# Optimization experiments

Hardware: AMD Instinct MI355X
Metric: run time of the kernel (lower is better)

The kernel has to match this reference:

```python
import jax, jax.numpy as jnp
import numpy as np

T, B, D, H = 256, 64, 1024, 1024


def _linear_params(key, fan_in, shape_w, shape_b):
    kw, kb = jax.random.split(key)
    bound = 1.0 / np.sqrt(fan_in)
    W = jax.random.uniform(kw, shape_w, jnp.float32, -bound, bound)
    b = jax.random.uniform(kb, shape_b, jnp.float32, -bound, bound)
    return W, b


def setup_inputs() -> dict:
    key = jax.random.key(0)
    ks = jax.random.split(key, 6)
    x = jax.random.normal(ks[0], (T, B, D), jnp.float32)
    hidden = jnp.zeros((B, H), jnp.float32)
    cell = jnp.zeros((B, H), jnp.float32)
    W_in, b_in = _linear_params(ks[1], D, (H, D), (H,))
    W_hid, b_hid = _linear_params(ks[2], H, (H, H), (H,))
    # 4 gates (i, f, g, o), each with an x-path and h-path hidden->hidden Linear
    Wx_g, bx_g = _linear_params(ks[3], H, (4, H, H), (4, H))
    Wh_g, bh_g = _linear_params(ks[4], H, (4, H, H), (4, H))
    return {"x": x, "hidden": hidden, "cell": cell,
            "W_in": W_in, "b_in": b_in, "W_hid": W_hid, "b_hid": b_hid,
            "Wx_g": Wx_g, "bx_g": bx_g, "Wh_g": Wh_g, "bh_g": bh_g}


def reference(x, hidden, cell, W_in, b_in, W_hid, b_hid, Wx_g, bx_g, Wh_g, bh_g):
    # input_layer / hidden_layer projections, then 4 gate Linears per path,
    # mirroring the many-small-Linear LSTM cell of the torch module.
    def step(carry, x_t):
        h, c = carry
        x2h = x_t @ W_in.T + b_in          # [B, H]
        h2h = h @ W_hid.T + b_hid          # [B, H]
        g = (jnp.einsum('ghk,bk->gbh', Wx_g, x2h) + bx_g[:, None, :]
             + jnp.einsum('ghk,bk->gbh', Wh_g, h2h) + bh_g[:, None, :])  # [4, B, H]
        i = jax.nn.sigmoid(g[0])
        f = jax.nn.sigmoid(g[1])
        gg = jnp.tanh(g[2])
        o = jax.nn.sigmoid(g[3])
        c_new = f * c + i * gg
        h_new = o * jnp.tanh(c_new)
        return (h_new, c_new), None

    (h, c), _ = jax.lax.scan(step, (hidden, cell), x)
    return (h, c)
```

## Files before the change

### kernel.cpp

```cpp
#include <hip/hip_runtime.h>

typedef __attribute__((ext_vector_type(8))) short short8;
typedef __attribute__((ext_vector_type(4))) float f32x4;

#define SEQ_BLOCKS 64

__device__ __forceinline__ unsigned short f2bf(float f) {
  unsigned u = __float_as_uint(f);
  u = u + 0x7fffu + ((u >> 16) & 1u);
  return (unsigned short)(u >> 16);
}
__device__ __forceinline__ unsigned short f2h(float f) {
  _Float16 h = (_Float16)f;
  unsigned short r;
  __builtin_memcpy(&r, &h, 2);
  return r;
}
__device__ __forceinline__ float h2f(unsigned short u) {
  _Float16 h;
  __builtin_memcpy(&h, &u, 2);
  return (float)h;
}
__device__ __forceinline__ void gload16(const void* g, void* l) {
  __builtin_amdgcn_global_load_lds(
      (const __attribute__((address_space(1))) unsigned int*)g,
      (__attribute__((address_space(3))) unsigned int*)l, 16, 0, 0);
}
__device__ __forceinline__ float fast_sigmoid(float x) {
  return 1.0f / (1.0f + __expf(-x));
}
__device__ __forceinline__ float fast_tanh(float x) {
  return 2.0f / (1.0f + __expf(-2.0f * x)) - 1.0f;
}

__global__ void k_conv_bf16(const float* __restrict__ in, unsigned short* __restrict__ out) {
  size_t i = ((size_t)blockIdx.x * 256 + threadIdx.x) * 4;
  float4 v = *(const float4*)(in + i);
  unsigned short o[4] = {f2bf(v.x), f2bf(v.y), f2bf(v.z), f2bf(v.w)};
  *(uint2*)(out + i) = *(const uint2*)o;
}

__global__ void k_h0t(const float* __restrict__ hidden, unsigned short* __restrict__ hT) {
  int sb = blockIdx.x;
  int row = threadIdx.x >> 2, c4 = (threadIdx.x & 3) * 4;
  float4 v = *(const float4*)(hidden + (size_t)row * 1024 + sb * 16 + c4);
  unsigned short o[4] = {f2bf(v.x), f2bf(v.y), f2bf(v.z), f2bf(v.w)};
  unsigned long long u;
  __builtin_memcpy(&u, o, 8);
  *(unsigned long long*)(hT + (size_t)sb * 1024 + row * 16 + c4) = u;
}

__global__ void k_transpose(const float* __restrict__ in, unsigned short* __restrict__ out,
                            int R, int C) {
  __shared__ float tile[32][33];
  int bx = blockIdx.x * 32, by = blockIdx.y * 32;
  int tx = threadIdx.x & 31, ty = threadIdx.x >> 5;
  for (int i = 0; i < 32; i += 8)
    tile[ty + i][tx] = in[(size_t)(by + ty + i) * C + bx + tx];
  __syncthreads();
  for (int i = 0; i < 32; i += 8)
    out[(size_t)(bx + ty + i) * R + by + tx] = f2bf(tile[tx][ty + i]);
}

template<int OUTMODE>
__global__ __launch_bounds__(256) void k_gemm_bt(
    const unsigned short* __restrict__ A, const unsigned short* __restrict__ B,
    unsigned short* __restrict__ C, const float* __restrict__ bias,
    int M, int N, int K) {
  __shared__ unsigned short As[128 * 32];
  __shared__ unsigned short Bs[128 * 32];
  const int tid = threadIdx.x;
  const int wv = tid >> 6, l = tid & 63;
  const int m0 = blockIdx.y * 128, n0 = blockIdx.x * 128;
  const int wr = (wv >> 1) * 64, wc = (wv & 1) * 64;
  f32x4 acc[4][4] = {};
  for (int k0 = 0; k0 < K; k0 += 32) {
#pragma unroll
    for (int j = 0; j < 2; ++j) {
      int c = wv * 128 + j * 64 + l;
      int row = c >> 2, kc = (c & 3) * 8;
      gload16(A + (size_t)(m0 + row) * K + k0 + kc, (char*)As + c * 16);
      gload16(B + (size_t)(n0 + row) * K + k0 + kc, (char*)Bs + c * 16);
    }
    __syncthreads();
    short8 af[4], bfr[4];
#pragma unroll
    for (int rf = 0; rf < 4; ++rf)
      af[rf] = *(const short8*)(As + (wr + rf * 16 + (l & 15)) * 32 + (l >> 4) * 8);
#pragma unroll
    for (int cf = 0; cf < 4; ++cf)
      bfr[cf] = *(const short8*)(Bs + (wc + cf * 16 + (l & 15)) * 32 + (l >> 4) * 8);
#pragma unroll
    for (int rf = 0; rf < 4; ++rf)
#pragma unroll
      for (int cf = 0; cf < 4; ++cf)
        acc[rf][cf] = __builtin_amdgcn_mfma_f32_16x16x32_bf16(af[rf], bfr[cf], acc[rf][cf], 0, 0, 0);
    __syncthreads();
  }
#pragma unroll
  for (int cf = 0; cf < 4; ++cf) {
    int col = n0 + wc + cf * 16 + (l & 15);
    float bv = bias ? bias[col] : 0.0f;
#pragma unroll
    for (int rf = 0; rf < 4; ++rf) {
#pragma unroll
      for (int i = 0; i < 4; ++i) {
        int row = m0 + wr + rf * 16 + (l >> 4) * 4 + i;
        float v = acc[rf][cf][i] + bv;
        if (OUTMODE == 0) {
          C[(size_t)row * N + col] = f2bf(v);
        } else {
          int t = row >> 6, b = row & 63;
          int g = col >> 10, c = col & 1023;
          size_t idx = (size_t)(t * 64 + (c >> 4)) * 4096 + (g * 64 + b) * 16 + (c & 15);
          C[idx] = f2h(v);
        }
      }
    }
  }
}

__global__ void k_bias(const float* __restrict__ Wxg, const float* __restrict__ bxg,
                       const float* __restrict__ b_in, const float* __restrict__ Whg,
                       const float* __restrict__ bhg, const float* __restrict__ b_hid,
                       float* __restrict__ gbias) {
  int col = blockIdx.x * 64 + (threadIdx.x >> 2);
  int p = threadIdx.x & 3;
  const float* wx = Wxg + (size_t)col * 1024;
  const float* wh = Whg + (size_t)col * 1024;
  float s = 0.f;
  for (int k = p * 256; k < p * 256 + 256; ++k)
    s += wx[k] * b_in[k] + wh[k] * b_hid[k];
  s += __shfl_down(s, 2, 4);
  s += __shfl_down(s, 1, 4);
  if (p == 0) gbias[col] = s + bxg[col] + bhg[col];
}

__global__ __launch_bounds__(256, 1) void k_lstm_seq(
    const unsigned short* __restrict__ GX2,
    const unsigned short* __restrict__ Whc,
    const float* __restrict__ cell,
    unsigned short* __restrict__ hstep,
    float* __restrict__ out,
    unsigned* __restrict__ flags) {
  __shared__ float pbuf[34816];
  const int tid = threadIdx.x;
  const int wv = tid >> 6, l = tid & 63;
  const int bid = blockIdx.x;
  const int a = l & 15, q = l >> 4;

  short8 w[4][8];
#pragma unroll
  for (int ct = 0; ct < 4; ++ct)
#pragma unroll
    for (int u = 0; u < 8; ++u)
      w[ct][u] = *(const short8*)(
          Whc + (size_t)(ct * 1024 + bid * 16 + a) * 1024 + wv * 256 + u * 32 + q * 8);

  const int eb = tid >> 2;
  const int ej = (tid & 3) * 4;
  float c_reg[4];
  {
    float4 c4 = *(const float4*)(cell + (size_t)eb * 1024 + bid * 16 + ej);
    c_reg[0] = c4.x; c_reg[1] = c4.y; c_reg[2] = c4.z; c_reg[3] = c4.w;
  }

  const size_t abase = (size_t)(wv * 16 + (q >> 1)) * 1024 + a * 16 + (q & 1) * 8;
  const unsigned* pollp = flags + wv * 32 + a;

  for (int t = 0; t < 256; ++t) {
    const unsigned short* chunk = GX2 + ((size_t)t * 64 + bid) * 4096;
    unsigned long long gxu[4];
#pragma unroll
    for (int g = 0; g < 4; ++g)
      gxu[g] = *(const unsigned long long*)(chunk + (g * 64 + eb) * 16 + ej);

    if (t > 0) {
      const unsigned tgt = (unsigned)t;
      for (;;) {
        unsigned v = __hip_atomic_load(pollp, __ATOMIC_RELAXED, __HIP_MEMORY_SCOPE_AGENT);
        if (__all((int)(v >= tgt))) break;
        __builtin_amdgcn_s_sleep(1);
      }
      __builtin_amdgcn_fence(__ATOMIC_ACQUIRE, "workgroup");
      __builtin_amdgcn_sched_barrier(0);
    }

    const unsigned short* hb = hstep + ((size_t)t << 16) + abase;
    short8 afr[4][8];
#pragma unroll
    for (int u = 0; u < 8; ++u)
#pragma unroll
      for (int rt = 0; rt < 4; ++rt)
        afr[rt][u] = *(const short8*)(hb + u * 2048 + rt * 256);

    f32x4 acc[4][4] = {};
#pragma unroll
    for (int u = 0; u < 8; ++u)
#pragma unroll
      for (int rt = 0; rt < 4; ++rt)
#pragma unroll
        for (int ct = 0; ct < 4; ++ct)
          acc[rt][ct] = __builtin_amdgcn_mfma_f32_16x16x32_bf16(afr[rt][u], w[ct][u],
                                                                acc[rt][ct], 0, 0, 0);

    const int pb = (t & 1) * 17408 + wv * 4352;
#pragma unroll
    for (int rt = 0; rt < 4; ++rt)
#pragma unroll
      for (int ct = 0; ct < 4; ++ct) {
        int gc = a * 4 + ct;
        int b0 = (rt * 16 + q * 4) ^ ((((gc) >> 3) & 3) << 2);
        *(f32x4*)&pbuf[pb + gc * 68 + b0] = acc[rt][ct];
      }
    __syncthreads();

    const int pr = (t & 1) * 17408;
    float sg[4][4];
#pragma unroll
    for (int g = 0; g < 4; ++g) {
      unsigned short gx4[4];
      __builtin_memcpy(gx4, &gxu[g], 8);
#pragma unroll
      for (int i = 0; i < 4; ++i) {
        int gc = (ej + i) * 4 + g;
        int bx = eb ^ ((((gc) >> 3) & 3) << 2);
        float s = pbuf[pr + 0 * 4352 + gc * 68 + bx] + pbuf[pr + 1 * 4352 + gc * 68 + bx] +
                  pbuf[pr + 2 * 4352 + gc * 68 + bx] + pbuf[pr + 3 * 4352 + gc * 68 + bx];
        sg[g][i] = s + h2f(gx4[i]);
      }
    }
    float hnew[4];
#pragma unroll
    for (int i = 0; i < 4; ++i) {
      float ig = fast_sigmoid(sg[0][i]);
      float fg = fast_sigmoid(sg[1][i]);
      float gg = fast_tanh(sg[2][i]);
      float og = fast_sigmoid(sg[3][i]);
      c_reg[i] = fg * c_reg[i] + ig * gg;
      hnew[i] = og * fast_tanh(c_reg[i]);
    }

    if (t == 255) {
      float4 h4 = {hnew[0], hnew[1], hnew[2], hnew[3]};
      float4 c4 = {c_reg[0], c_reg[1], c_reg[2], c_reg[3]};
      *(float4*)(out + (size_t)eb * 1024 + bid * 16 + ej) = h4;
      *(float4*)(out + 65536 + (size_t)eb * 1024 + bid * 16 + ej) = c4;
    } else {
      unsigned short hs[4] = {f2bf(hnew[0]), f2bf(hnew[1]), f2bf(hnew[2]), f2bf(hnew[3])};
      unsigned long long hv;
      __builtin_memcpy(&hv, hs, 8);
      __hip_atomic_store(
          (unsigned long long*)(hstep + ((size_t)(t + 1) << 16) + (size_t)bid * 1024 +
                                eb * 16 + ej),
          hv, __ATOMIC_RELAXED, __HIP_MEMORY_SCOPE_AGENT);
      asm volatile("s_waitcnt vmcnt(0)" ::: "memory");
      __syncthreads();
      if (tid == 0)
        __hip_atomic_store(&flags[(bid >> 4) * 32 + (bid & 15)], (unsigned)(t + 1),
                           __ATOMIC_RELAXED, __HIP_MEMORY_SCOPE_AGENT);
    }
  }
}

extern "C" void kernel_launch(void* const* d_in, const int* in_sizes, int n_in,
                              void* d_out, int out_size, void* d_ws, size_t ws_size,
                              hipStream_t stream) {
  const float* x      = (const float*)d_in[0];
  const float* hidden = (const float*)d_in[1];
  const float* cell   = (const float*)d_in[2];
  const float* W_in   = (const float*)d_in[3];
  const float* b_in   = (const float*)d_in[4];
  const float* W_hid  = (const float*)d_in[5];
  const float* b_hid  = (const float*)d_in[6];
  const float* Wx_g   = (const float*)d_in[7];
  const float* bx_g   = (const float*)d_in[8];
  const float* Wh_g   = (const float*)d_in[9];
  const float* bh_g   = (const float*)d_in[10];
  float* out = (float*)d_out;

  char* ws = (char*)d_ws;
  unsigned short* GX2   = (unsigned short*)(ws);
  unsigned short* Xbf   = (unsigned short*)(ws + 134217728);
  unsigned short* WxGb  = (unsigned short*)(ws + 167772160);
  unsigned short* WhGb  = (unsigned short*)(ws + 176160768);
  unsigned short* WinT  = (unsigned short*)(ws + 184549376);
  unsigned short* WhidT = (unsigned short*)(ws + 186646528);
  unsigned short* Wxc   = (unsigned short*)(ws + 188743680);
  unsigned short* Whc   = (unsigned short*)(ws + 197132288);
  float*          gbias = (float*)(ws + 205520896);
  unsigned short* hstep = (unsigned short*)(ws + 134217728);
  unsigned*       flags = (unsigned*)(ws + 184549376);

  k_conv_bf16<<<16384, 256, 0, stream>>>(x, Xbf);
  k_conv_bf16<<<4096, 256, 0, stream>>>(Wx_g, WxGb);
  k_conv_bf16<<<4096, 256, 0, stream>>>(Wh_g, WhGb);
  k_transpose<<<dim3(32, 32), 256, 0, stream>>>(W_in, WinT, 1024, 1024);
  k_transpose<<<dim3(32, 32), 256, 0, stream>>>(W_hid, WhidT, 1024, 1024);
  k_gemm_bt<0><<<dim3(8, 32), 256, 0, stream>>>(WxGb, WinT, Wxc, nullptr, 4096, 1024, 1024);
  k_gemm_bt<0><<<dim3(8, 32), 256, 0, stream>>>(WhGb, WhidT, Whc, nullptr, 4096, 1024, 1024);
  k_bias<<<64, 256, 0, stream>>>(Wx_g, bx_g, b_in, Wh_g, bh_g, b_hid, gbias);
  k_gemm_bt<1><<<dim3(32, 128), 256, 0, stream>>>(Xbf, Wxc, GX2, gbias, 16384, 4096, 1024);
  k_h0t<<<64, 256, 0, stream>>>(hidden, hstep);
  hipMemsetAsync(flags, 0, 512, stream);
  k_lstm_seq<<<SEQ_BLOCKS, 256, 0, stream>>>(GX2, Whc, cell, hstep, out, flags);
}
```

Measured before the change: 2.166 ms.

## Fuse input-projection GEMM into the sequential LSTM kernel per timestep

Drops the large precomputed x-path gate GEMM and its fp16 gate buffer. Each sequential block now loads the bf16 x rows and the combined x-weights and runs the x-path MFMAs inside every timestep, adding the folded bias from registers. This removes a full-GPU GEMM and the large write and read of its output. In exchange it roughly doubles the per-step MFMA work on the 64-block critical path and greatly raises register pressure from extra resident weight and fragment arrays, so spills are likely.

```diff
diff --git a/kernel.cpp b/kernel.cpp
--- a/kernel.cpp
+++ b/kernel.cpp
@@ -9,12 +9,6 @@
   unsigned u = __float_as_uint(f);
   u = u + 0x7fffu + ((u >> 16) & 1u);
   return (unsigned short)(u >> 16);
-}
-__device__ __forceinline__ unsigned short f2h(float f) {
-  _Float16 h = (_Float16)f;
-  unsigned short r;
-  __builtin_memcpy(&r, &h, 2);
-  return r;
 }
 __device__ __forceinline__ float h2f(unsigned short u) {
   _Float16 h;
@@ -62,11 +56,9 @@
     out[(size_t)(bx + ty + i) * R + by + tx] = f2bf(tile[tx][ty + i]);
 }
 
-template<int OUTMODE>
 __global__ __launch_bounds__(256) void k_gemm_bt(
     const unsigned short* __restrict__ A, const unsigned short* __restrict__ B,
-    unsigned short* __restrict__ C, const float* __restrict__ bias,
-    int M, int N, int K) {
+    unsigned short* __restrict__ C, int M, int N, int K) {
   __shared__ unsigned short As[128 * 32];
   __shared__ unsigned short Bs[128 * 32];
   const int tid = threadIdx.x;
@@ -100,21 +92,12 @@
 #pragma unroll
   for (int cf = 0; cf < 4; ++cf) {
     int col = n0 + wc + cf * 16 + (l & 15);
-    float bv = bias ? bias[col] : 0.0f;
 #pragma unroll
     for (int rf = 0; rf < 4; ++rf) {
 #pragma unroll
       for (int i = 0; i < 4; ++i) {
         int row = m0 + wr + rf * 16 + (l >> 4) * 4 + i;
-        float v = acc[rf][cf][i] + bv;
-        if (OUTMODE == 0) {
-          C[(size_t)row * N + col] = f2bf(v);
-        } else {
-          int t = row >> 6, b = row & 63;
-          int g = col >> 10, c = col & 1023;
-          size_t idx = (size_t)(t * 64 + (c >> 4)) * 4096 + (g * 64 + b) * 16 + (c & 15);
-          C[idx] = f2h(v);
-        }
+        C[(size_t)row * N + col] = f2bf(acc[rf][cf][i]);
       }
     }
   }
@@ -137,8 +120,10 @@
 }
 
 __global__ __launch_bounds__(256, 1) void k_lstm_seq(
-    const unsigned short* __restrict__ GX2,
+    const unsigned short* __restrict__ Xbf,
+    const unsigned short* __restrict__ Wxc,
     const unsigned short* __restrict__ Whc,
+    const float* __restrict__ gbias,
     const float* __restrict__ cell,
     unsigned short* __restrict__ hstep,
     float* __restrict__ out,
@@ -149,13 +134,15 @@
   const int bid = blockIdx.x;
   const int a = l & 15, q = l >> 4;
 
-  short8 w[4][8];
+  short8 wh[4][8], wx[4][8];
 #pragma unroll
   for (int ct = 0; ct < 4; ++ct)
 #pragma unroll
-    for (int u = 0; u < 8; ++u)
-      w[ct][u] = *(const short8*)(
-          Whc + (size_t)(ct * 1024 + bid * 16 + a) * 1024 + wv * 256 + u * 32 + q * 8);
+    for (int u = 0; u < 8; ++u) {
+      size_t off = (size_t)(ct * 1024 + bid * 16 + a) * 1024 + wv * 256 + u * 32 + q * 8;
+      wh[ct][u] = *(const short8*)(Whc + off);
+      wx[ct][u] = *(const short8*)(Wxc + off);
+    }
 
   const int eb = tid >> 2;
   const int ej = (tid & 3) * 4;
@@ -164,16 +151,24 @@
     float4 c4 = *(const float4*)(cell + (size_t)eb * 1024 + bid * 16 + ej);
     c_reg[0] = c4.x; c_reg[1] = c4.y; c_reg[2] = c4.z; c_reg[3] = c4.w;
   }
+  float gb[4][4];
+#pragma unroll
+  for (int g = 0; g < 4; ++g)
+#pragma unroll
+    for (int i = 0; i < 4; ++i)
+      gb[g][i] = gbias[g * 1024 + bid * 16 + ej + i];
 
   const size_t abase = (size_t)(wv * 16 + (q >> 1)) * 1024 + a * 16 + (q & 1) * 8;
   const unsigned* pollp = flags + wv * 32 + a;
 
   for (int t = 0; t < 256; ++t) {
-    const unsigned short* chunk = GX2 + ((size_t)t * 64 + bid) * 4096;
-    unsigned long long gxu[4];
-#pragma unroll
-    for (int g = 0; g < 4; ++g)
-      gxu[g] = *(const unsigned long long*)(chunk + (g * 64 + eb) * 16 + ej);
+    const unsigned short* xb = Xbf + ((size_t)t << 16) + (size_t)a * 1024 + wv * 256 + q * 8;
+    short8 afx[4][8];
+#pragma unroll
+    for (int u = 0; u < 8; ++u)
+#pragma unroll
+      for (int rt = 0; rt < 4; ++rt)
+        afx[rt][u] = *(const short8*)(xb + (size_t)rt * 16384 + u * 32);
 
     if (t > 0) {
       const unsigned tgt = (unsigned)t;
@@ -201,7 +196,15 @@
       for (int rt = 0; rt < 4; ++rt)
 #pragma unroll
         for (int ct = 0; ct < 4; ++ct)
-          acc[rt][ct] = __builtin_amdgcn_mfma_f32_16x16x32_bf16(afr[rt][u], w[ct][u],
+          acc[rt][ct] = __builtin_amdgcn_mfma_f32_16x16x32_bf16(afx[rt][u], wx[ct][u],
+                                                                acc[rt][ct], 0, 0, 0);
+#pragma unroll
+    for (int u = 0; u < 8; ++u)
+#pragma unroll
+      for (int rt = 0; rt < 4; ++rt)
+#pragma unroll
+        for (int ct = 0; ct < 4; ++ct)
+          acc[rt][ct] = __builtin_amdgcn_mfma_f32_16x16x32_bf16(afr[rt][u], wh[ct][u],
                                                                 acc[rt][ct], 0, 0, 0);
 
     const int pb = (t & 1) * 17408 + wv * 4352;
@@ -219,15 +222,13 @@
     float sg[4][4];
 #pragma unroll
     for (int g = 0; g < 4; ++g) {
-      unsigned short gx4[4];
-      __builtin_memcpy(gx4, &gxu[g], 8);
 #pragma unroll
       for (int i = 0; i < 4; ++i) {
         int gc = (ej + i) * 4 + g;
         int bx = eb ^ ((((gc) >> 3) & 3) << 2);
         float s = pbuf[pr + 0 * 4352 + gc * 68 + bx] + pbuf[pr + 1 * 4352 + gc * 68 + bx] +
                   pbuf[pr + 2 * 4352 + gc * 68 + bx] + pbuf[pr + 3 * 4352 + gc * 68 + bx];
-        sg[g][i] = s + h2f(gx4[i]);
+        sg[g][i] = s + gb[g][i];
       }
     }
     float hnew[4];
@@ -280,7 +281,7 @@
   float* out = (float*)d_out;
 
   char* ws = (char*)d_ws;
-  unsigned short* GX2   = (unsigned short*)(ws);
+  unsigned short* hstep = (unsigned short*)(ws);
   unsigned short* Xbf   = (unsigned short*)(ws + 134217728);
   unsigned short* WxGb  = (unsigned short*)(ws + 167772160);
   unsigned short* WhGb  = (unsigned short*)(ws + 176160768);
@@ -289,7 +290,6 @@
   unsigned short* Wxc   = (unsigned short*)(ws + 188743680);
   unsigned short* Whc   = (unsigned short*)(ws + 197132288);
   float*          gbias = (float*)(ws + 205520896);
-  unsigned short* hstep = (unsigned short*)(ws + 134217728);
   unsigned*       flags = (unsigned*)(ws + 184549376);
 
   k_conv_bf16<<<16384, 256, 0, stream>>>(x, Xbf);
@@ -297,11 +297,10 @@
   k_conv_bf16<<<4096, 256, 0, stream>>>(Wh_g, WhGb);
   k_transpose<<<dim3(32, 32), 256, 0, stream>>>(W_in, WinT, 1024, 1024);
   k_transpose<<<dim3(32, 32), 256, 0, stream>>>(W_hid, WhidT, 1024, 1024);
-  k_gemm_bt<0><<<dim3(8, 32), 256, 0, stream>>>(WxGb, WinT, Wxc, nullptr, 4096, 1024, 1024);
-  k_gemm_bt<0><<<dim3(8, 32), 256, 0, stream>>>(WhGb, WhidT, Whc, nullptr, 4096, 1024, 1024);
+  k_gemm_bt<<<dim3(8, 32), 256, 0, stream>>>(WxGb, WinT, Wxc, 4096, 1024, 1024);
+  k_gemm_bt<<<dim3(8, 32), 256, 0, stream>>>(WhGb, WhidT, Whc, 4096, 1024, 1024);
   k_bias<<<64, 256, 0, stream>>>(Wx_g, bx_g, b_in, Wh_g, bh_g, b_hid, gbias);
-  k_gemm_bt<1><<<dim3(32, 128), 256, 0, stream>>>(Xbf, Wxc, GX2, gbias, 16384, 4096, 1024);
   k_h0t<<<64, 256, 0, stream>>>(hidden, hstep);
   hipMemsetAsync(flags, 0, 512, stream);
-  k_lstm_seq<<<SEQ_BLOCKS, 256, 0, stream>>>(GX2, Whc, cell, hstep, out, flags);
-}
+  k_lstm_seq<<<SEQ_BLOCKS, 256, 0, stream>>>(Xbf, Wxc, Whc, gbias, cell, hstep, out, flags);
+}
```

After: 2.945 ms. +36.0%, slower.
